# Optimization experiments

Measured on AMD Instinct MI355X. Metric: run time of the kernel, lower is better.

## Reference

```python
import jax, jax.numpy as jnp
import numpy as np

D_K = 256

def setup_inputs() -> dict:
    key = jax.random.key(0)
    k1, k2, k3, k4 = jax.random.split(key, 4)
    B, S, D = 4, 4096, 256
    x = jax.random.normal(k1, (B, S, D), dtype=jnp.float32)
    scale = 1.0 / np.sqrt(D)
    W_q = jax.random.normal(k2, (D, D_K), dtype=jnp.float32) * scale
    W_k = jax.random.normal(k3, (D, D_K), dtype=jnp.float32) * scale
    W_v = jax.random.normal(k4, (D, D_K), dtype=jnp.float32) * scale
    return {"x": x, "W_q": W_q, "W_k": W_k, "W_v": W_v}

def reference(x, W_q, W_k, W_v):
    # x: [B, S, D]; weights: [D, d_k]
    B, S, D = x.shape
    Q = jnp.einsum('bsd,dk->bsk', x, W_q)
    K = jnp.einsum('bsd,dk->bsk', x, W_k)
    V = jnp.einsum('bsd,dk->bsk', x, W_v)
    scores = jnp.einsum('bqk,bsk->bqs', Q, K) / jnp.sqrt(jnp.float32(D_K))  # [B, S, S]
    causal = jnp.tril(jnp.ones((S, S), dtype=bool))
    scores = jnp.where(causal[None, :, :], scores, -jnp.inf)
    weights = jax.nn.softmax(scores, axis=-1)
    return jnp.einsum('bqs,bsk->bqk', weights, V)
```

## Files before the change

### kernel.cpp

```cpp
#include <hip/hip_runtime.h>
#include <hip/hip_bf16.h>
#include <cstdint>


typedef __bf16 b8v __attribute__((ext_vector_type(8)));
typedef __bf16 b4v __attribute__((ext_vector_type(4)));
typedef float  f4v __attribute__((ext_vector_type(4)));
typedef float  f16v __attribute__((ext_vector_type(16)));
typedef int    i4v __attribute__((ext_vector_type(4)));
typedef int    i2v __attribute__((ext_vector_type(2)));

#define MFMA16(a, b, c) __builtin_amdgcn_mfma_f32_16x16x32_bf16((a), (b), (c), 0, 0, 0)
#define MFMA32(a, b, c) __builtin_amdgcn_mfma_f32_32x32x16_bf16((a), (b), (c), 0, 0, 0)

#define GLOAD_LDS(gsrc, ldst)                                                        \
  __builtin_amdgcn_global_load_lds((const __attribute__((address_space(1))) void*)(gsrc), \
                                   (__attribute__((address_space(3))) void*)(ldst), 16, 0, 0)

#define SCALE_Q 0.09016844005f
#define MASKVAL -3.0e38f

static constexpr int DT = 20;

static constexpr size_t WS_WT = 0;
static constexpr size_t WS_Q  = 524288;
static constexpr size_t WS_K  = WS_Q + 8388608;
static constexpr size_t WS_VT = WS_K + 8388608;

__global__ void prep_wt(const float* __restrict__ Wq, const float* __restrict__ Wk,
                        const float* __restrict__ Wv, __bf16* __restrict__ wt) {
  int gid = blockIdx.x * blockDim.x + threadIdx.x;
  int w = gid >> 16, rem = gid & 65535;
  int c = rem >> 8, d = rem & 255;
  const float* W = (w == 0) ? Wq : (w == 1) ? Wk : Wv;
  float v = W[d * 256 + c];
  if (w == 0) v *= SCALE_Q;
  wt[gid] = (__bf16)v;
}

__global__ void __launch_bounds__(256, 2) proj_qkv(
    const float* __restrict__ x, const __bf16* __restrict__ wt,
    __bf16* __restrict__ Qw, __bf16* __restrict__ Kw, __bf16* __restrict__ Vt) {
  __shared__ __bf16 w_lds[64][264];
  __shared__ __bf16 v_lds[64][72];
  const int tid = threadIdx.x;
  const int wv = tid >> 6, lane = tid & 63, c = lane & 15, g = lane >> 4;
  const int ww = blockIdx.x >> 8, rb = blockIdx.x & 255;
  const int rowbase = rb * 64;
  const int batch = rb >> 6, sblk = rb & 63;

  b8v xf[8];
  {
    const float* xr = x + (size_t)(rowbase + wv * 16 + c) * 256;
#pragma unroll
    for (int ks = 0; ks < 8; ++ks) {
      const float4 a0 = *reinterpret_cast<const float4*>(xr + 32 * ks + 8 * g);
      const float4 a1 = *reinterpret_cast<const float4*>(xr + 32 * ks + 8 * g + 4);
      b8v f;
      f[0] = (__bf16)a0.x; f[1] = (__bf16)a0.y; f[2] = (__bf16)a0.z; f[3] = (__bf16)a0.w;
      f[4] = (__bf16)a1.x; f[5] = (__bf16)a1.y; f[6] = (__bf16)a1.z; f[7] = (__bf16)a1.w;
      xf[ks] = f;
    }
  }
  for (int ct = 0; ct < 4; ++ct) {
    __syncthreads();
    {
      const int srow = tid >> 2, sch = tid & 3;
      const i4v* src = reinterpret_cast<const i4v*>(
          wt + ((size_t)(ww * 256 + ct * 64 + srow)) * 256 + sch * 64);
      i4v* dst = reinterpret_cast<i4v*>(&w_lds[srow][sch * 64]);
#pragma unroll
      for (int j = 0; j < 8; ++j) dst[j] = src[j];
    }
    __syncthreads();
    f4v pacc[4];
#pragma unroll
    for (int i = 0; i < 4; ++i) pacc[i] = (f4v){0.f, 0.f, 0.f, 0.f};
#pragma unroll
    for (int ks = 0; ks < 8; ++ks) {
#pragma unroll
      for (int nf = 0; nf < 4; ++nf) {
        b8v wf = *reinterpret_cast<const b8v*>(&w_lds[16 * nf + c][32 * ks + 8 * g]);
        pacc[nf] = MFMA16(xf[ks], wf, pacc[nf]);
      }
    }
    if (ww < 2) {
      __bf16* o = (ww == 0) ? Qw : Kw;
      const int row0 = rowbase + wv * 16 + 4 * g;
#pragma unroll
      for (int nf = 0; nf < 4; ++nf) {
        const int col = ct * 64 + 16 * nf + c;
#pragma unroll
        for (int r = 0; r < 4; ++r)
          o[(size_t)(row0 + r) * 256 + col] = (__bf16)pacc[nf][r];
      }
    } else {
      const int sp = 16 * wv + 4 * g;
#pragma unroll
      for (int nf = 0; nf < 4; ++nf) {
        b4v pk;
        pk[0] = (__bf16)pacc[nf][0]; pk[1] = (__bf16)pacc[nf][1];
        pk[2] = (__bf16)pacc[nf][2]; pk[3] = (__bf16)pacc[nf][3];
        *reinterpret_cast<b4v*>(&v_lds[16 * nf + c][sp]) = pk;
      }
      __syncthreads();
      {
        const int dd = tid >> 2, ch = tid & 3;
        const b8v* sp8 = reinterpret_cast<const b8v*>(&v_lds[dd][ch * 16]);
        __bf16* dst =
            Vt + ((size_t)(batch * 256 + ct * 64 + dd)) * 4096 + sblk * 64 + ch * 16;
        reinterpret_cast<b8v*>(dst)[0] = sp8[0];
        reinterpret_cast<b8v*>(dst)[1] = sp8[1];
      }
    }
  }
}

__global__ void __launch_bounds__(512, 2) attn_fwd(
    const __bf16* __restrict__ Qw, const __bf16* __restrict__ Kw,
    const __bf16* __restrict__ Vt, float* __restrict__ out,
    float* __restrict__ lsum_buf, int CB) {
  extern __shared__ char smem[];
  const int tid = threadIdx.x;
  const int wv = tid >> 6, lane = tid & 63;
  const int q5 = lane & 31, hi = lane >> 5;

  const int p = blockIdx.x;
  const int bb = p & 3;
  const int slot = p >> 2;
  if (slot >= CB) return;

  int Q = 0, acc0 = 0, c = 1;
  for (; Q < 16; ++Q) {
    const int T_ = 8 * Q + 8;
    c = (T_ + DT - 1) / DT;
    if (acc0 + c > slot) break;
    acc0 += c;
  }
  const int j = slot - acc0;
  const int T = 8 * Q + 8;
  const int ta = j * T / c, tb = (j + 1) * T / c;
  const bool single = (c == 1);

  const __bf16* Kg = Kw + (size_t)bb * 4096 * 256;
  const __bf16* Vg = Vt + (size_t)bb * 256 * 4096;

  auto stage = [&](int sb, int tt) {
    char* Kd = smem + sb * 32768;
    char* Vd = Kd + 16384;
#pragma unroll
    for (int i = 0; i < 2; ++i) {
      const int n = i * 512 + tid;
      const int r = n >> 5, cp = n & 31;
      const __bf16* src = Kg + (size_t)(tt * 32 + r) * 256 + ((cp ^ r) << 3);
      GLOAD_LDS(src, Kd + ((i * 512 + wv * 64) << 4));
    }
#pragma unroll
    for (int i = 0; i < 2; ++i) {
      const int n = i * 512 + tid;
      const int d = n >> 2, cp = n & 3;
      const __bf16* src =
          Vg + (size_t)d * 4096 + tt * 32 + ((cp ^ ((d >> 3) & 3)) << 3);
      GLOAD_LDS(src, Vd + ((i * 512 + wv * 64) << 4));
    }
  };

  b8v qf[16];
  {
    const __bf16* qr =
        Qw + ((size_t)(bb * 4096 + Q * 256 + wv * 32 + q5)) * 256 + 8 * hi;
#pragma unroll
    for (int ks = 0; ks < 16; ++ks)
      qf[ks] = *reinterpret_cast<const b8v*>(qr + ks * 16);
  }

  f16v acc[8];
#pragma unroll
  for (int i = 0; i < 8; ++i)
#pragma unroll
    for (int jj = 0; jj < 16; ++jj) acc[i][jj] = 0.f;
  float lsum = 0.f;
  const int qg = Q * 256 + wv * 32 + q5;

  stage(0, ta);
  __syncthreads();

  for (int tt = ta; tt < tb; ++tt) {
    const int cur = (tt - ta) & 1;
    if (tt + 1 < tb) stage(cur ^ 1, tt + 1);

    f16v sv;
#pragma unroll
    for (int jj = 0; jj < 16; ++jj) sv[jj] = 0.f;
    const char* kb0 = smem + cur * 32768 + q5 * 512;
    __builtin_amdgcn_s_setprio(1);
#pragma unroll
    for (int ks = 0; ks < 16; ++ks) {
      const int co = (((ks << 1) | hi) ^ q5) << 4;
      const b8v k0 = *reinterpret_cast<const b8v*>(kb0 + co);
      sv = MFMA32(k0, qf[ks], sv);
    }
    __builtin_amdgcn_s_setprio(0);

    if (tt * 32 + 31 > Q * 256 + wv * 32) {
#pragma unroll
      for (int reg = 0; reg < 16; ++reg) {
        const int R = (reg & 3) + 8 * (reg >> 2) + 4 * hi;
        if (tt * 32 + R > qg) sv[reg] = MASKVAL;
      }
    }
#pragma unroll
    for (int jj = 0; jj < 16; ++jj) sv[jj] = exp2f(sv[jj]);
    {
      float u0 = 0.f, u1s = 0.f, u2 = 0.f, u3 = 0.f;
#pragma unroll
      for (int jj = 0; jj < 16; jj += 4) {
        u0 += sv[jj]; u1s += sv[jj + 1]; u2 += sv[jj + 2]; u3 += sv[jj + 3];
      }
      lsum += (u0 + u1s) + (u2 + u3);
    }
    unsigned a0[4], a1[4];
#pragma unroll
    for (int mb = 0; mb < 4; ++mb) {
      b4v pk;
      pk[0] = (__bf16)sv[4 * mb]; pk[1] = (__bf16)sv[4 * mb + 1];
      pk[2] = (__bf16)sv[4 * mb + 2]; pk[3] = (__bf16)sv[4 * mb + 3];
      const uint2 uu = *reinterpret_cast<uint2*>(&pk);
      a0[mb] = uu.x; a1[mb] = uu.y;
    }
    const char* vbase = smem + cur * 32768 + 16384 + q5 * 64;
#pragma unroll
    for (int ks = 0; ks < 2; ++ks) {
      i4v wi;
#if __has_builtin(__builtin_amdgcn_permlane32_swap)
      const i2v e0 = __builtin_amdgcn_permlane32_swap((int)a0[2 * ks],
                                                      (int)a0[2 * ks + 1], false, false);
      const i2v e1 = __builtin_amdgcn_permlane32_swap((int)a1[2 * ks],
                                                      (int)a1[2 * ks + 1], false, false);
      wi[0] = e0[0]; wi[1] = e1[0]; wi[2] = e0[1]; wi[3] = e1[1];
#else
      const unsigned x0 = (unsigned)__shfl_xor((int)a0[2 * ks], 32);
      const unsigned x1 = (unsigned)__shfl_xor((int)a1[2 * ks], 32);
      const unsigned y0 = (unsigned)__shfl_xor((int)a0[2 * ks + 1], 32);
      const unsigned y1 = (unsigned)__shfl_xor((int)a1[2 * ks + 1], 32);
      wi[0] = hi ? (int)y0 : (int)a0[2 * ks];
      wi[1] = hi ? (int)y1 : (int)a1[2 * ks];
      wi[2] = hi ? (int)a0[2 * ks + 1] : (int)x0;
      wi[3] = hi ? (int)a1[2 * ks + 1] : (int)x1;
#endif
      const b8v pa = *reinterpret_cast<b8v*>(&wi);
      const int cov = ((((ks << 1) | hi)) ^ ((q5 >> 3) & 3)) << 4;
      __builtin_amdgcn_s_setprio(1);
#pragma unroll
      for (int db = 0; db < 8; ++db) {
        const b8v vf = *reinterpret_cast<const b8v*>(vbase + db * 2048 + cov);
        acc[db] = MFMA32(pa, vf, acc[db]);
      }
      __builtin_amdgcn_s_setprio(0);
    }
    __syncthreads();
  }

  lsum += __shfl_xor(lsum, 32);
  if (single) {
    const float inv = 1.f / lsum;
#pragma unroll
    for (int reg = 0; reg < 16; ++reg) {
      const int R = (reg & 3) + 8 * (reg >> 2) + 4 * hi;
      const float ivr = __shfl(inv, R);
      float* orow = out + ((size_t)(bb * 4096 + Q * 256 + wv * 32 + R)) * 256 + q5;
#pragma unroll
      for (int db = 0; db < 8; ++db) orow[db * 32] = acc[db][reg] * ivr;
    }
  } else {
#pragma unroll
    for (int reg = 0; reg < 16; ++reg) {
      const int R = (reg & 3) + 8 * (reg >> 2) + 4 * hi;
      float* orow = out + ((size_t)(bb * 4096 + Q * 256 + wv * 32 + R)) * 256 + q5;
#pragma unroll
      for (int db = 0; db < 8; ++db) atomicAdd(&orow[db * 32], acc[db][reg]);
    }
    if (hi == 0)
      atomicAdd(&lsum_buf[(size_t)bb * 4096 + Q * 256 + wv * 32 + q5], lsum);
  }
}

__global__ void __launch_bounds__(256) combine_k(float* __restrict__ out,
                                                 const float* __restrict__ lsum_buf) {
  const int row = blockIdx.x * 32 + (threadIdx.x >> 3);
  const int Q = (row >> 8) & 15;
  if (8 * Q + 8 <= DT) return;
  const float inv = 1.f / lsum_buf[row];
  float* dst = out + (size_t)row * 256 + (threadIdx.x & 7) * 32;
#pragma unroll
  for (int k = 0; k < 8; ++k) {
    f4v v = reinterpret_cast<const f4v*>(dst)[k];
    reinterpret_cast<f4v*>(dst)[k] = v * inv;
  }
}

extern "C" void kernel_launch(void* const* d_in, const int* in_sizes, int n_in,
                              void* d_out, int out_size, void* d_ws, size_t ws_size,
                              hipStream_t stream) {
  const float* x  = reinterpret_cast<const float*>(d_in[0]);
  const float* Wq = reinterpret_cast<const float*>(d_in[1]);
  const float* Wk = reinterpret_cast<const float*>(d_in[2]);
  const float* Wv = reinterpret_cast<const float*>(d_in[3]);
  char* ws = reinterpret_cast<char*>(d_ws);
  __bf16* wt = reinterpret_cast<__bf16*>(ws + WS_WT);
  __bf16* Qw = reinterpret_cast<__bf16*>(ws + WS_Q);
  __bf16* Kw = reinterpret_cast<__bf16*>(ws + WS_K);
  __bf16* Vt = reinterpret_cast<__bf16*>(ws + WS_VT);
  float* lsum_buf = reinterpret_cast<float*>(ws);
  float* out = reinterpret_cast<float*>(d_out);

  int CB = 0;
  for (int Q = 0; Q < 16; ++Q) CB += (8 * Q + 8 + DT - 1) / DT;

  (void)hipMemsetAsync(d_out, 0, (size_t)out_size * 4, stream);
  prep_wt<<<768, 256, 0, stream>>>(Wq, Wk, Wv, wt);
  proj_qkv<<<768, 256, 0, stream>>>(x, wt, Qw, Kw, Vt);
  (void)hipMemsetAsync(lsum_buf, 0, 4 * 4096 * sizeof(float), stream);

  constexpr int kSmem = 65536;
  (void)hipFuncSetAttribute(reinterpret_cast<const void*>(attn_fwd),
                            hipFuncAttributeMaxDynamicSharedMemorySize, kSmem);
  attn_fwd<<<4 * 64, 512, kSmem, stream>>>(Qw, Kw, Vt, out, lsum_buf, CB);
  combine_k<<<512, 256, 0, stream>>>(out, lsum_buf);
}
```

Baseline: 138.4 us.

## Double attention KV tile to 64 keys and use async swizzled LDS loads in projection

The attention kernel now stages 64-key K/V tiles per double-buffer stage (128 KB LDS) and processes each as two 32-key halves, with new swizzle patterns and rescaled split bookkeeping (DT=10 over 64-key tiles). This is meant to halve the number of barriers and pipeline steps per block and give the loads more time to overlap with compute. Separately, the projection kernel loads its weight tiles through global_load_lds with an XOR-swizzled layout instead of copying them through registers. The larger LDS footprint limits attention occupancy to one block per CU, and the swizzle indexing has to match exactly.

```diff
diff --git a/kernel.cpp b/kernel.cpp
--- a/kernel.cpp
+++ b/kernel.cpp
@@ -20,7 +20,7 @@
 #define SCALE_Q 0.09016844005f
 #define MASKVAL -3.0e38f
 
-static constexpr int DT = 20;
+static constexpr int DT = 10;
 
 static constexpr size_t WS_WT = 0;
 static constexpr size_t WS_Q  = 524288;
@@ -41,7 +41,7 @@
 __global__ void __launch_bounds__(256, 2) proj_qkv(
     const float* __restrict__ x, const __bf16* __restrict__ wt,
     __bf16* __restrict__ Qw, __bf16* __restrict__ Kw, __bf16* __restrict__ Vt) {
-  __shared__ __bf16 w_lds[64][264];
+  __shared__ __bf16 w_lds[16384];
   __shared__ __bf16 v_lds[64][72];
   const int tid = threadIdx.x;
   const int wv = tid >> 6, lane = tid & 63, c = lane & 15, g = lane >> 4;
@@ -62,15 +62,18 @@
       xf[ks] = f;
     }
   }
+  const __bf16* wbase = wt + (size_t)ww * 65536;
+  char* wl = reinterpret_cast<char*>(w_lds);
   for (int ct = 0; ct < 4; ++ct) {
     __syncthreads();
     {
-      const int srow = tid >> 2, sch = tid & 3;
-      const i4v* src = reinterpret_cast<const i4v*>(
-          wt + ((size_t)(ww * 256 + ct * 64 + srow)) * 256 + sch * 64);
-      i4v* dst = reinterpret_cast<i4v*>(&w_lds[srow][sch * 64]);
-#pragma unroll
-      for (int j = 0; j < 8; ++j) dst[j] = src[j];
+#pragma unroll
+      for (int i = 0; i < 8; ++i) {
+        const int n = i * 256 + tid;
+        const int r = n >> 5, cp = n & 31;
+        const __bf16* src = wbase + (size_t)(ct * 64 + r) * 256 + ((cp ^ (r & 7)) << 3);
+        GLOAD_LDS(src, wl + ((i * 256 + wv * 64) << 4));
+      }
     }
     __syncthreads();
     f4v pacc[4];
@@ -80,7 +83,8 @@
     for (int ks = 0; ks < 8; ++ks) {
 #pragma unroll
       for (int nf = 0; nf < 4; ++nf) {
-        b8v wf = *reinterpret_cast<const b8v*>(&w_lds[16 * nf + c][32 * ks + 8 * g]);
+        const b8v wf = *reinterpret_cast<const b8v*>(
+            wl + (16 * nf + c) * 512 + (((4 * ks + g) ^ (c & 7)) << 4));
         pacc[nf] = MFMA16(xf[ks], wf, pacc[nf]);
       }
     }
@@ -132,35 +136,35 @@
 
   int Q = 0, acc0 = 0, c = 1;
   for (; Q < 16; ++Q) {
-    const int T_ = 8 * Q + 8;
+    const int T_ = 4 * Q + 4;
     c = (T_ + DT - 1) / DT;
     if (acc0 + c > slot) break;
     acc0 += c;
   }
   const int j = slot - acc0;
-  const int T = 8 * Q + 8;
+  const int T = 4 * Q + 4;
   const int ta = j * T / c, tb = (j + 1) * T / c;
   const bool single = (c == 1);
 
   const __bf16* Kg = Kw + (size_t)bb * 4096 * 256;
   const __bf16* Vg = Vt + (size_t)bb * 256 * 4096;
 
-  auto stage = [&](int sb, int tt) {
-    char* Kd = smem + sb * 32768;
-    char* Vd = Kd + 16384;
-#pragma unroll
-    for (int i = 0; i < 2; ++i) {
+  auto stage = [&](int s, int tt) {
+    char* Kd = smem + s * 65536;
+    char* Vd = Kd + 32768;
+#pragma unroll
+    for (int i = 0; i < 4; ++i) {
       const int n = i * 512 + tid;
       const int r = n >> 5, cp = n & 31;
-      const __bf16* src = Kg + (size_t)(tt * 32 + r) * 256 + ((cp ^ r) << 3);
+      const __bf16* src = Kg + (size_t)(tt * 64 + r) * 256 + ((cp ^ (r & 31)) << 3);
       GLOAD_LDS(src, Kd + ((i * 512 + wv * 64) << 4));
     }
 #pragma unroll
-    for (int i = 0; i < 2; ++i) {
+    for (int i = 0; i < 4; ++i) {
       const int n = i * 512 + tid;
-      const int d = n >> 2, cp = n & 3;
+      const int d = n >> 3, cp = n & 7;
       const __bf16* src =
-          Vg + (size_t)d * 4096 + tt * 32 + ((cp ^ ((d >> 3) & 3)) << 3);
+          Vg + (size_t)d * 4096 + tt * 64 + ((cp ^ ((d >> 1) & 7)) << 3);
       GLOAD_LDS(src, Vd + ((i * 512 + wv * 64) << 4));
     }
   };
@@ -189,74 +193,78 @@
     const int cur = (tt - ta) & 1;
     if (tt + 1 < tb) stage(cur ^ 1, tt + 1);
 
-    f16v sv;
-#pragma unroll
-    for (int jj = 0; jj < 16; ++jj) sv[jj] = 0.f;
-    const char* kb0 = smem + cur * 32768 + q5 * 512;
-    __builtin_amdgcn_s_setprio(1);
-#pragma unroll
-    for (int ks = 0; ks < 16; ++ks) {
-      const int co = (((ks << 1) | hi) ^ q5) << 4;
-      const b8v k0 = *reinterpret_cast<const b8v*>(kb0 + co);
-      sv = MFMA32(k0, qf[ks], sv);
-    }
-    __builtin_amdgcn_s_setprio(0);
-
-    if (tt * 32 + 31 > Q * 256 + wv * 32) {
-#pragma unroll
-      for (int reg = 0; reg < 16; ++reg) {
-        const int R = (reg & 3) + 8 * (reg >> 2) + 4 * hi;
-        if (tt * 32 + R > qg) sv[reg] = MASKVAL;
-      }
-    }
-#pragma unroll
-    for (int jj = 0; jj < 16; ++jj) sv[jj] = exp2f(sv[jj]);
-    {
-      float u0 = 0.f, u1s = 0.f, u2 = 0.f, u3 = 0.f;
-#pragma unroll
-      for (int jj = 0; jj < 16; jj += 4) {
-        u0 += sv[jj]; u1s += sv[jj + 1]; u2 += sv[jj + 2]; u3 += sv[jj + 3];
-      }
-      lsum += (u0 + u1s) + (u2 + u3);
-    }
-    unsigned a0[4], a1[4];
-#pragma unroll
-    for (int mb = 0; mb < 4; ++mb) {
-      b4v pk;
-      pk[0] = (__bf16)sv[4 * mb]; pk[1] = (__bf16)sv[4 * mb + 1];
-      pk[2] = (__bf16)sv[4 * mb + 2]; pk[3] = (__bf16)sv[4 * mb + 3];
-      const uint2 uu = *reinterpret_cast<uint2*>(&pk);
-      a0[mb] = uu.x; a1[mb] = uu.y;
-    }
-    const char* vbase = smem + cur * 32768 + 16384 + q5 * 64;
-#pragma unroll
-    for (int ks = 0; ks < 2; ++ks) {
-      i4v wi;
+#pragma unroll
+    for (int h = 0; h < 2; ++h) {
+      f16v sv;
+#pragma unroll
+      for (int jj = 0; jj < 16; ++jj) sv[jj] = 0.f;
+      const char* kb0 = smem + cur * 65536 + (h * 32 + q5) * 512;
+      __builtin_amdgcn_s_setprio(1);
+#pragma unroll
+      for (int ks = 0; ks < 16; ++ks) {
+        const int co = (((ks << 1) | hi) ^ q5) << 4;
+        const b8v k0 = *reinterpret_cast<const b8v*>(kb0 + co);
+        sv = MFMA32(k0, qf[ks], sv);
+      }
+      __builtin_amdgcn_s_setprio(0);
+
+      const int kbase = tt * 64 + h * 32;
+      if (kbase + 31 > Q * 256 + wv * 32) {
+#pragma unroll
+        for (int reg = 0; reg < 16; ++reg) {
+          const int R = (reg & 3) + 8 * (reg >> 2) + 4 * hi;
+          if (kbase + R > qg) sv[reg] = MASKVAL;
+        }
+      }
+#pragma unroll
+      for (int jj = 0; jj < 16; ++jj) sv[jj] = exp2f(sv[jj]);
+      {
+        float u0 = 0.f, u1s = 0.f, u2 = 0.f, u3 = 0.f;
+#pragma unroll
+        for (int jj = 0; jj < 16; jj += 4) {
+          u0 += sv[jj]; u1s += sv[jj + 1]; u2 += sv[jj + 2]; u3 += sv[jj + 3];
+        }
+        lsum += (u0 + u1s) + (u2 + u3);
+      }
+      unsigned a0[4], a1[4];
+#pragma unroll
+      for (int mb = 0; mb < 4; ++mb) {
+        b4v pk;
+        pk[0] = (__bf16)sv[4 * mb]; pk[1] = (__bf16)sv[4 * mb + 1];
+        pk[2] = (__bf16)sv[4 * mb + 2]; pk[3] = (__bf16)sv[4 * mb + 3];
+        const uint2 uu = *reinterpret_cast<uint2*>(&pk);
+        a0[mb] = uu.x; a1[mb] = uu.y;
+      }
+      const char* vb = smem + cur * 65536 + 32768 + q5 * 128;
+#pragma unroll
+      for (int ks = 0; ks < 2; ++ks) {
+        i4v wi;
 #if __has_builtin(__builtin_amdgcn_permlane32_swap)
-      const i2v e0 = __builtin_amdgcn_permlane32_swap((int)a0[2 * ks],
-                                                      (int)a0[2 * ks + 1], false, false);
-      const i2v e1 = __builtin_amdgcn_permlane32_swap((int)a1[2 * ks],
-                                                      (int)a1[2 * ks + 1], false, false);
-      wi[0] = e0[0]; wi[1] = e1[0]; wi[2] = e0[1]; wi[3] = e1[1];
+        const i2v e0 = __builtin_amdgcn_permlane32_swap((int)a0[2 * ks],
+                                                        (int)a0[2 * ks + 1], false, false);
+        const i2v e1 = __builtin_amdgcn_permlane32_swap((int)a1[2 * ks],
+                                                        (int)a1[2 * ks + 1], false, false);
+        wi[0] = e0[0]; wi[1] = e1[0]; wi[2] = e0[1]; wi[3] = e1[1];
 #else
-      const unsigned x0 = (unsigned)__shfl_xor((int)a0[2 * ks], 32);
-      const unsigned x1 = (unsigned)__shfl_xor((int)a1[2 * ks], 32);
-      const unsigned y0 = (unsigned)__shfl_xor((int)a0[2 * ks + 1], 32);
-      const unsigned y1 = (unsigned)__shfl_xor((int)a1[2 * ks + 1], 32);
-      wi[0] = hi ? (int)y0 : (int)a0[2 * ks];
-      wi[1] = hi ? (int)y1 : (int)a1[2 * ks];
-      wi[2] = hi ? (int)a0[2 * ks + 1] : (int)x0;
-      wi[3] = hi ? (int)a1[2 * ks + 1] : (int)x1;
+        const unsigned x0 = (unsigned)__shfl_xor((int)a0[2 * ks], 32);
+        const unsigned x1 = (unsigned)__shfl_xor((int)a1[2 * ks], 32);
+        const unsigned y0 = (unsigned)__shfl_xor((int)a0[2 * ks + 1], 32);
+        const unsigned y1 = (unsigned)__shfl_xor((int)a1[2 * ks + 1], 32);
+        wi[0] = hi ? (int)y0 : (int)a0[2 * ks];
+        wi[1] = hi ? (int)y1 : (int)a1[2 * ks];
+        wi[2] = hi ? (int)a0[2 * ks + 1] : (int)x0;
+        wi[3] = hi ? (int)a1[2 * ks + 1] : (int)x1;
 #endif
-      const b8v pa = *reinterpret_cast<b8v*>(&wi);
-      const int cov = ((((ks << 1) | hi)) ^ ((q5 >> 3) & 3)) << 4;
-      __builtin_amdgcn_s_setprio(1);
-#pragma unroll
-      for (int db = 0; db < 8; ++db) {
-        const b8v vf = *reinterpret_cast<const b8v*>(vbase + db * 2048 + cov);
-        acc[db] = MFMA32(pa, vf, acc[db]);
-      }
-      __builtin_amdgcn_s_setprio(0);
+        const b8v pa = *reinterpret_cast<b8v*>(&wi);
+        const int cov = (((h << 2) | (ks << 1) | hi) ^ ((q5 >> 1) & 7)) << 4;
+        __builtin_amdgcn_s_setprio(1);
+#pragma unroll
+        for (int db = 0; db < 8; ++db) {
+          const b8v vf = *reinterpret_cast<const b8v*>(vb + db * 4096 + cov);
+          acc[db] = MFMA32(pa, vf, acc[db]);
+        }
+        __builtin_amdgcn_s_setprio(0);
+      }
     }
     __syncthreads();
   }
@@ -289,7 +297,7 @@
                                                  const float* __restrict__ lsum_buf) {
   const int row = blockIdx.x * 32 + (threadIdx.x >> 3);
   const int Q = (row >> 8) & 15;
-  if (8 * Q + 8 <= DT) return;
+  if (4 * Q + 4 <= DT) return;
   const float inv = 1.f / lsum_buf[row];
   float* dst = out + (size_t)row * 256 + (threadIdx.x & 7) * 32;
 #pragma unroll
@@ -315,14 +323,14 @@
   float* out = reinterpret_cast<float*>(d_out);
 
   int CB = 0;
-  for (int Q = 0; Q < 16; ++Q) CB += (8 * Q + 8 + DT - 1) / DT;
+  for (int Q = 0; Q < 16; ++Q) CB += (4 * Q + 4 + DT - 1) / DT;
 
   (void)hipMemsetAsync(d_out, 0, (size_t)out_size * 4, stream);
   prep_wt<<<768, 256, 0, stream>>>(Wq, Wk, Wv, wt);
   proj_qkv<<<768, 256, 0, stream>>>(x, wt, Qw, Kw, Vt);
   (void)hipMemsetAsync(lsum_buf, 0, 4 * 4096 * sizeof(float), stream);
 
-  constexpr int kSmem = 65536;
+  constexpr int kSmem = 131072;
   (void)hipFuncSetAttribute(reinterpret_cast<const void*>(attn_fwd),
                             hipFuncAttributeMaxDynamicSharedMemorySize, kSmem);
   attn_fwd<<<4 * 64, 512, kSmem, stream>>>(Qw, Kw, Vt, out, lsum_buf, CB);
```

After: 165.1 us. 19.3% more time.

## Fuse split-KV normalization into attention via last-block counter, drop combine kernel

Applied to the files above, without the earlier changes.

Removes the separate combine kernel by having the last block to finish each split query segment, detected with an atomic counter, normalize that segment's output rows in place. It also narrows the output memset to the rows that receive atomic accumulation, moves the lsum memset ahead of the projections alongside the counter reset, and launches exactly 4*CB blocks. This saves a kernel launch and a full memset pass over the output, at the cost of a serialized tail inside the last block using scalar atomic loads.

```diff
diff --git a/kernel.cpp b/kernel.cpp
--- a/kernel.cpp
+++ b/kernel.cpp
@@ -22,10 +22,12 @@
 
 static constexpr int DT = 20;
 
-static constexpr size_t WS_WT = 0;
-static constexpr size_t WS_Q  = 524288;
-static constexpr size_t WS_K  = WS_Q + 8388608;
-static constexpr size_t WS_VT = WS_K + 8388608;
+static constexpr size_t WS_WT   = 0;
+static constexpr size_t WS_LSUM = 393216;
+static constexpr size_t WS_CNT  = 458752;
+static constexpr size_t WS_Q    = 524288;
+static constexpr size_t WS_K    = WS_Q + 8388608;
+static constexpr size_t WS_VT   = WS_K + 8388608;
 
 __global__ void prep_wt(const float* __restrict__ Wq, const float* __restrict__ Wk,
                         const float* __restrict__ Wv, __bf16* __restrict__ wt) {
@@ -119,8 +121,9 @@
 __global__ void __launch_bounds__(512, 2) attn_fwd(
     const __bf16* __restrict__ Qw, const __bf16* __restrict__ Kw,
     const __bf16* __restrict__ Vt, float* __restrict__ out,
-    float* __restrict__ lsum_buf, int CB) {
+    float* __restrict__ lsum_buf, int* __restrict__ seg_cnt, int CB) {
   extern __shared__ char smem[];
+  __shared__ int lastFlag;
   const int tid = threadIdx.x;
   const int wv = tid >> 6, lane = tid & 63;
   const int q5 = lane & 31, hi = lane >> 5;
@@ -272,30 +275,36 @@
 #pragma unroll
       for (int db = 0; db < 8; ++db) orow[db * 32] = acc[db][reg] * ivr;
     }
-  } else {
-#pragma unroll
-    for (int reg = 0; reg < 16; ++reg) {
-      const int R = (reg & 3) + 8 * (reg >> 2) + 4 * hi;
-      float* orow = out + ((size_t)(bb * 4096 + Q * 256 + wv * 32 + R)) * 256 + q5;
-#pragma unroll
-      for (int db = 0; db < 8; ++db) atomicAdd(&orow[db * 32], acc[db][reg]);
-    }
-    if (hi == 0)
-      atomicAdd(&lsum_buf[(size_t)bb * 4096 + Q * 256 + wv * 32 + q5], lsum);
-  }
-}
-
-__global__ void __launch_bounds__(256) combine_k(float* __restrict__ out,
-                                                 const float* __restrict__ lsum_buf) {
-  const int row = blockIdx.x * 32 + (threadIdx.x >> 3);
-  const int Q = (row >> 8) & 15;
-  if (8 * Q + 8 <= DT) return;
-  const float inv = 1.f / lsum_buf[row];
-  float* dst = out + (size_t)row * 256 + (threadIdx.x & 7) * 32;
-#pragma unroll
-  for (int k = 0; k < 8; ++k) {
-    f4v v = reinterpret_cast<const f4v*>(dst)[k];
-    reinterpret_cast<f4v*>(dst)[k] = v * inv;
+    return;
+  }
+#pragma unroll
+  for (int reg = 0; reg < 16; ++reg) {
+    const int R = (reg & 3) + 8 * (reg >> 2) + 4 * hi;
+    float* orow = out + ((size_t)(bb * 4096 + Q * 256 + wv * 32 + R)) * 256 + q5;
+#pragma unroll
+    for (int db = 0; db < 8; ++db) atomicAdd(&orow[db * 32], acc[db][reg]);
+  }
+  if (hi == 0)
+    atomicAdd(&lsum_buf[(size_t)bb * 4096 + Q * 256 + wv * 32 + q5], lsum);
+
+  __syncthreads();
+  __threadfence();
+  if (tid == 0) lastFlag = (atomicAdd(&seg_cnt[bb * 16 + Q], 1) == c - 1);
+  __syncthreads();
+  if (lastFlag) {
+    __threadfence();
+    const int row = tid >> 1;
+    const int col0 = (tid & 1) * 128;
+    const size_t grow = (size_t)(bb * 4096 + Q * 256 + row);
+    const float inv =
+        1.f / __hip_atomic_load(&lsum_buf[grow], __ATOMIC_RELAXED,
+                                __HIP_MEMORY_SCOPE_AGENT);
+    float* dst = out + grow * 256 + col0;
+    for (int k = 0; k < 128; ++k) {
+      const float v = __hip_atomic_load(&dst[k], __ATOMIC_RELAXED,
+                                        __HIP_MEMORY_SCOPE_AGENT);
+      dst[k] = v * inv;
+    }
   }
 }
 
@@ -311,20 +320,23 @@
   __bf16* Qw = reinterpret_cast<__bf16*>(ws + WS_Q);
   __bf16* Kw = reinterpret_cast<__bf16*>(ws + WS_K);
   __bf16* Vt = reinterpret_cast<__bf16*>(ws + WS_VT);
-  float* lsum_buf = reinterpret_cast<float*>(ws);
+  float* lsum_buf = reinterpret_cast<float*>(ws + WS_LSUM);
+  int* seg_cnt = reinterpret_cast<int*>(ws + WS_CNT);
   float* out = reinterpret_cast<float*>(d_out);
 
   int CB = 0;
   for (int Q = 0; Q < 16; ++Q) CB += (8 * Q + 8 + DT - 1) / DT;
 
-  (void)hipMemsetAsync(d_out, 0, (size_t)out_size * 4, stream);
+  for (int b = 0; b < 4; ++b)
+    (void)hipMemsetAsync(out + ((size_t)b * 4096 + 512) * 256, 0,
+                         (size_t)3584 * 256 * 4, stream);
+  (void)hipMemsetAsync(lsum_buf, 0, 65536 + 256, stream);
+
   prep_wt<<<768, 256, 0, stream>>>(Wq, Wk, Wv, wt);
   proj_qkv<<<768, 256, 0, stream>>>(x, wt, Qw, Kw, Vt);
-  (void)hipMemsetAsync(lsum_buf, 0, 4 * 4096 * sizeof(float), stream);
 
   constexpr int kSmem = 65536;
   (void)hipFuncSetAttribute(reinterpret_cast<const void*>(attn_fwd),
                             hipFuncAttributeMaxDynamicSharedMemorySize, kSmem);
-  attn_fwd<<<4 * 64, 512, kSmem, stream>>>(Qw, Kw, Vt, out, lsum_buf, CB);
-  combine_k<<<512, 256, 0, stream>>>(out, lsum_buf);
+  attn_fwd<<<4 * CB, 512, kSmem, stream>>>(Qw, Kw, Vt, out, lsum_buf, seg_cnt, CB);
 }
```

Result: slower. 378.4 us (+173.4%).
